# Performance work log

Measured on AMD Instinct MI355X. Metric: run time of the kernel, lower is better.

The kernel has to match this reference:

```python
import jax, jax.numpy as jnp
import numpy as np

N_NODES = 100000
N_EDGES = 1600000
D_IN = 128
D_HID = 128
N_LAYERS = 3


def setup_inputs() -> dict:
    key = jax.random.key(0)
    ks = jax.random.split(key, 7)
    x = jax.random.normal(ks[0], (N_NODES, D_IN), dtype=jnp.float32)
    edge_index = jax.random.randint(ks[1], (2, N_EDGES), 0, N_NODES, dtype=jnp.int32)
    s = 1.0 / np.sqrt(D_HID)
    # stacked per-layer MLP params: lin1 (in->h), lin2 (h->h); in==h==128 for all layers
    W1 = jax.random.uniform(ks[2], (N_LAYERS, D_IN, D_HID), jnp.float32, -s, s)
    b1 = jax.random.uniform(ks[3], (N_LAYERS, D_HID), jnp.float32, -s, s)
    W2 = jax.random.uniform(ks[4], (N_LAYERS, D_HID, D_HID), jnp.float32, -s, s)
    b2 = jax.random.uniform(ks[5], (N_LAYERS, D_HID), jnp.float32, -s, s)
    return {"x": x, "edge_index": edge_index, "W1": W1, "b1": b1, "W2": W2, "b2": b2}


def _gin_layer(x, src, dst, W1, b1, W2, b2):
    # GINConv: out = MLP((1+eps)*x + sum_{j in N(i)} x_j), eps = 0
    agg = jax.ops.segment_sum(x[src], dst, num_segments=N_NODES)  # [N, C]
    h = x + agg
    h = jnp.maximum(h @ W1 + b1, 0.0)  # MLP internal ReLU
    return h @ W2 + b2


def reference(x, edge_index, W1, b1, W2, b2):
    src, dst = edge_index[0], edge_index[1]
    for i in range(N_LAYERS):
        x = _gin_layer(x, src, dst, W1[i], b1[i], W2[i], b2[i])
        if i < N_LAYERS - 1:  # inter-layer act (norm=Identity, dropout=0)
            x = jnp.maximum(x, 0.0)
    return x
```

## Files before the change

### kernel.cpp

```cpp
#include <hip/hip_runtime.h>
#include <hip/hip_bf16.h>

#define D 128

typedef float f32x4 __attribute__((ext_vector_type(4)));
typedef __bf16 bf16x8 __attribute__((ext_vector_type(8)));

__device__ __forceinline__ unsigned short f2bf(float f) {
  unsigned int u = __float_as_uint(f);
  u += 0x7fff + ((u >> 16) & 1);
  return (unsigned short)(u >> 16);
}

__device__ __forceinline__ void gl_lds16(const void* g, void* l) {
  __builtin_amdgcn_global_load_lds(
      (const __attribute__((address_space(1))) unsigned int*)g,
      (__attribute__((address_space(3))) unsigned int*)l, 16, 0, 0);
}

__device__ __forceinline__ int wave_incl_scan(int v, int lane) {
#pragma unroll
  for (int d = 1; d < 64; d <<= 1) {
    int t = __shfl_up(v, d);
    if (lane >= d) v += t;
  }
  return v;
}

#define NBK 196
#define CHUNK 4096

__global__ __launch_bounds__(256) void k_bhist(const int* __restrict__ dst, int E,
                                               int* __restrict__ bcount) {
  __shared__ int cnt[NBK];
  const int tid = threadIdx.x;
  for (int i = tid; i < NBK; i += 256) cnt[i] = 0;
  __syncthreads();
  const int e0 = blockIdx.x * CHUNK;
  const int emax = min(e0 + CHUNK, E);
  for (int e = e0 + tid; e < emax; e += 256)
    atomicAdd(&cnt[((unsigned)dst[e]) >> 9], 1);
  __syncthreads();
  for (int i = tid; i < NBK; i += 256)
    if (cnt[i]) atomicAdd(&bcount[i], cnt[i]);
}

__global__ void k_bscan(const int* __restrict__ bcount, int* __restrict__ bucket_base) {
  int t = threadIdx.x;
  int lane = t & 63, w = t >> 6;
  int v = (t < NBK) ? bcount[t] : 0;
  int s = wave_incl_scan(v, lane);
  __shared__ int ws[4];
  if (lane == 63) ws[w] = s;
  __syncthreads();
  int off = 0;
  for (int i = 0; i < w; i++) off += ws[i];
  if (t < NBK) bucket_base[t] = off + s - v;
  if (t == 0) bucket_base[NBK] = ws[0] + ws[1] + ws[2] + ws[3];
}

__global__ __launch_bounds__(256) void k_binA(const int* __restrict__ src,
                                              const int* __restrict__ dst, int E,
                                              const int* __restrict__ bucket_base,
                                              int* __restrict__ bcursor,
                                              int* __restrict__ pairbuf) {
  __shared__ int cnt[NBK];
  __shared__ int base[NBK];
  const int tid = threadIdx.x;
  const int e0 = blockIdx.x * CHUNK;
  const int emax = min(e0 + CHUNK, E);
  for (int i = tid; i < NBK; i += 256) cnt[i] = 0;
  __syncthreads();
  for (int e = e0 + tid; e < emax; e += 256)
    atomicAdd(&cnt[((unsigned)dst[e]) >> 9], 1);
  __syncthreads();
  for (int i = tid; i < NBK; i += 256) {
    int c = cnt[i];
    int b = 0;
    if (c) b = atomicAdd(&bcursor[i], c) + bucket_base[i];
    base[i] = b;
    cnt[i] = 0;
  }
  __syncthreads();
  for (int e = e0 + tid; e < emax; e += 256) {
    int d = dst[e];
    int bk = ((unsigned)d) >> 9;
    int pos = base[bk] + atomicAdd(&cnt[bk], 1);
    pairbuf[pos] = (src[e] << 9) | (d & 511);
  }
}

#define SEG_CAP 12800
__global__ __launch_bounds__(256) void k_binB(const int* __restrict__ pairbuf,
                                              const int* __restrict__ bucket_base,
                                              int* __restrict__ col,
                                              int* __restrict__ row_ptr, int N) {
  __shared__ int sdeg[512];
  __shared__ int rpl[512];
  __shared__ int cur[512];
  __shared__ int wsum[4];
  __shared__ int stage[SEG_CAP];
  const int tid = threadIdx.x;
  const int lane = tid & 63, wid = tid >> 6;
  const int node0 = blockIdx.x << 9;
  const int nn = min(512, N - node0);
  const int start = bucket_base[blockIdx.x];
  const int end = bucket_base[blockIdx.x + 1];
  const int sz = end - start;
  for (int i = tid; i < 512; i += 256) { sdeg[i] = 0; cur[i] = 0; }
  __syncthreads();
  for (int i = tid; i < sz; i += 256)
    atomicAdd(&sdeg[pairbuf[start + i] & 511], 1);
  __syncthreads();
  int a = sdeg[2 * tid], b = sdeg[2 * tid + 1];
  int v = a + b;
  int s = wave_incl_scan(v, lane);
  if (lane == 63) wsum[wid] = s;
  __syncthreads();
  int off = 0;
  for (int k = 0; k < wid; k++) off += wsum[k];
  int e0l = off + s - v;
  rpl[2 * tid] = e0l;
  rpl[2 * tid + 1] = e0l + a;
  __syncthreads();
  for (int i = tid; i < nn; i += 256) row_ptr[node0 + i] = start + rpl[i];
  if (blockIdx.x == gridDim.x - 1 && tid == 0) row_ptr[N] = end;
  for (int i = tid; i < sz; i += 256) {
    int pk = pairbuf[start + i];
    int d = pk & 511;
    int pos = rpl[d] + atomicAdd(&cur[d], 1);
    if (pos < SEG_CAP) stage[pos] = (int)(((unsigned)pk) >> 9);
  }
  __syncthreads();
  for (int i = tid; i < sz; i += 256) col[start + i] = stage[i];
}

#define ISSUE8(vv, cvh, base)                              \
  _Pragma("unroll") for (int u = 0; u < 8; u++) {          \
    int s_ = __shfl((cvh), (base) + u);                    \
    vv[u] = Yu[(size_t)s_ * 64 + lane];                    \
  }

#define REDUCE8(vv, jb)                                    \
  _Pragma("unroll") for (int u = 0; u < 8; u++) {          \
    float fx_ = __uint_as_float(vv[u] << 16);              \
    float fy_ = __uint_as_float(vv[u] & 0xffff0000u);      \
    if ((jb) + u < degA) { axA += fx_; ayA += fy_; }       \
    else { axB += fx_; ayB += fy_; }                       \
  }

__global__ __launch_bounds__(256) void k_agg(const unsigned short* __restrict__ Y,
                                             const int* __restrict__ row_ptr,
                                             const int* __restrict__ col,
                                             const float* __restrict__ bias,
                                             unsigned short* __restrict__ H, int N) {
  const int pw = (blockIdx.x * 256 + threadIdx.x) >> 6;
  const int lane = threadIdx.x & 63;
  const int nA = pw * 2, nB = nA + 1;
  if (nA >= N) return;
  const bool hasB = (nB < N);
  const unsigned int* Yu = (const unsigned int*)Y;
  unsigned int svA = Yu[(size_t)nA * 64 + lane];
  unsigned int svB = hasB ? Yu[(size_t)nB * 64 + lane] : 0u;
  float2 bv = ((const float2*)bias)[lane];
  int rsA = row_ptr[nA];
  int reA = row_ptr[nA + 1];
  int reB = hasB ? row_ptr[nA + 2] : reA;
  rsA = __builtin_amdgcn_readfirstlane(rsA);
  reA = __builtin_amdgcn_readfirstlane(reA);
  reB = __builtin_amdgcn_readfirstlane(reB);
  const int degA = min(reA - rsA, 64);
  const int degB = min(reB - reA, 64);
  const int m = degA + degB;
  const int mPad = (m + 7) & ~7;
  const int nb = mPad >> 3;

  float axA = bv.x + __uint_as_float(svA << 16);
  float ayA = bv.y + __uint_as_float(svA & 0xffff0000u);
  float axB = bv.x + __uint_as_float(svB << 16);
  float ayB = bv.y + __uint_as_float(svB & 0xffff0000u);

  int cv0 = N, cv1 = N;
  if (lane < degA) cv0 = col[rsA + lane];
  else if (lane - degA < degB) cv0 = col[reA + (lane - degA)];
  if (64 + lane < m) cv1 = col[reA + (64 + lane - degA)];

  unsigned int b0[8], b1[8];
  int issued = 0, done = 0;
  if (nb > 0) { ISSUE8(b0, cv0, 0); issued = 1; }
  if (nb > 1) { ISSUE8(b1, cv0, 8); issued = 2; }
  while (done < nb) {
    if ((done & 1) == 0) { REDUCE8(b0, (done << 3)); }
    else { REDUCE8(b1, (done << 3)); }
    done++;
    if (issued < nb) {
      int ch = (issued < 8) ? cv0 : cv1;
      int bs = (issued & 7) << 3;
      if ((issued & 1) == 0) { ISSUE8(b0, ch, bs); }
      else { ISSUE8(b1, ch, bs); }
      issued++;
    }
  }
  for (int t = rsA + 64; t < reA; t++) {
    unsigned int v = Yu[(size_t)col[t] * 64 + lane];
    axA += __uint_as_float(v << 16);
    ayA += __uint_as_float(v & 0xffff0000u);
  }
  for (int t = reA + 64; t < reB; t++) {
    unsigned int v = Yu[(size_t)col[t] * 64 + lane];
    axB += __uint_as_float(v << 16);
    ayB += __uint_as_float(v & 0xffff0000u);
  }

  unsigned int pA = ((unsigned int)f2bf(fmaxf(ayA, 0.f)) << 16) | f2bf(fmaxf(axA, 0.f));
  ((unsigned int*)H)[(size_t)nA * 64 + lane] = pA;
  if (hasB) {
    unsigned int pB = ((unsigned int)f2bf(fmaxf(ayB, 0.f)) << 16) | f2bf(fmaxf(axB, 0.f));
    ((unsigned int*)H)[(size_t)nB * 64 + lane] = pB;
  }
}

__global__ void k_prep(const float* __restrict__ W1, const float* __restrict__ W2,
                       unsigned short* __restrict__ Wt) {
  int b = blockIdx.x;
  const float* W = (b & 1) ? (W2 + (size_t)(b >> 1) * D * D) : (W1 + (size_t)(b >> 1) * D * D);
  unsigned short* O = Wt + (size_t)b * D * D;
  for (int i = threadIdx.x; i < D * D; i += 256) {
    int n = i >> 7, k = i & 127;
    O[n * D + k] = f2bf(W[k * D + n]);
  }
}

template <bool A_FP32, bool OUT_FP32>
__global__ __launch_bounds__(256) void k_gemm(const void* __restrict__ Ain,
                                              const unsigned short* __restrict__ Wt,
                                              const float* __restrict__ bias,
                                              void* __restrict__ Cout, int M, int relu) {
  __shared__ __align__(16) unsigned short As[64 * 128];
  __shared__ __align__(16) unsigned short Bs[128 * 128];
  const int tid = threadIdx.x;
  const int wid = tid >> 6, lane = tid & 63;
  const int R0 = blockIdx.x * 64;

#pragma unroll
  for (int g = 0; g < 8; g++) {
    int flat = g * 256 + tid;
    int n = flat >> 4, p = flat & 15;
    int l = p ^ (n & 15);
    gl_lds16(Wt + (size_t)n * D + l * 8, &Bs[(size_t)(g * 256 + wid * 64) * 8]);
  }
  if (A_FP32) {
    const float* A = (const float*)Ain;
#pragma unroll
    for (int g = 0; g < 4; g++) {
      int flat = g * 256 + tid;
      int row = flat >> 4, p = flat & 15;
      int l = p ^ (row & 15);
      float4 a0 = make_float4(0.f, 0.f, 0.f, 0.f), a1 = a0;
      if (R0 + row < M) {
        a0 = *(const float4*)(A + (size_t)(R0 + row) * D + l * 8);
        a1 = *(const float4*)(A + (size_t)(R0 + row) * D + l * 8 + 4);
      }
      ushort4 v0, v1;
      v0.x = f2bf(a0.x); v0.y = f2bf(a0.y); v0.z = f2bf(a0.z); v0.w = f2bf(a0.w);
      v1.x = f2bf(a1.x); v1.y = f2bf(a1.y); v1.z = f2bf(a1.z); v1.w = f2bf(a1.w);
      *(ushort4*)&As[row * D + p * 8] = v0;
      *(ushort4*)&As[row * D + p * 8 + 4] = v1;
    }
  } else {
    const unsigned short* A = (const unsigned short*)Ain;
#pragma unroll
    for (int g = 0; g < 4; g++) {
      int flat = g * 256 + tid;
      int row = flat >> 4, p = flat & 15;
      int l = p ^ (row & 15);
      gl_lds16(A + (size_t)(R0 + row) * D + l * 8, &As[(size_t)(g * 256 + wid * 64) * 8]);
    }
  }
  __syncthreads();

  const int wr = wid >> 1, wc = wid & 1;
  const int lm = lane & 15, lq = lane >> 4;
  f32x4 acc[2][4];
#pragma unroll
  for (int i = 0; i < 2; i++)
#pragma unroll
    for (int j = 0; j < 4; j++) acc[i][j] = f32x4{0.f, 0.f, 0.f, 0.f};

#pragma unroll
  for (int kc = 0; kc < 4; kc++) {
    const int pc = (kc * 4 + lq) ^ lm;
    bf16x8 af[2], bfr[4];
#pragma unroll
    for (int i = 0; i < 2; i++)
      af[i] = *(const bf16x8*)&As[(wr * 32 + i * 16 + lm) * D + pc * 8];
#pragma unroll
    for (int j = 0; j < 4; j++)
      bfr[j] = *(const bf16x8*)&Bs[(wc * 64 + j * 16 + lm) * D + pc * 8];
#pragma unroll
    for (int i = 0; i < 2; i++)
#pragma unroll
      for (int j = 0; j < 4; j++)
        acc[i][j] = __builtin_amdgcn_mfma_f32_16x16x32_bf16(af[i], bfr[j], acc[i][j], 0, 0, 0);
  }

  float bv[4];
#pragma unroll
  for (int j = 0; j < 4; j++) bv[j] = bias ? bias[wc * 64 + j * 16 + lm] : 0.f;
#pragma unroll
  for (int i = 0; i < 2; i++) {
#pragma unroll
    for (int reg = 0; reg < 4; reg++) {
      const int gr = R0 + wr * 32 + i * 16 + lq * 4 + reg;
      if (gr < M) {
#pragma unroll
        for (int j = 0; j < 4; j++) {
          const int gc = wc * 64 + j * 16 + lm;
          float v = acc[i][j][reg] + bv[j];
          if (relu) v = fmaxf(v, 0.f);
          if (OUT_FP32)
            ((float*)Cout)[(size_t)gr * D + gc] = v;
          else
            ((unsigned short*)Cout)[(size_t)gr * D + gc] = f2bf(v);
        }
      }
    }
  }
}

__global__ __launch_bounds__(256) void k_gemm2(const unsigned short* __restrict__ Ain,
                                               const unsigned short* __restrict__ W2t,
                                               const unsigned short* __restrict__ W1t,
                                               const float* __restrict__ b2,
                                               unsigned short* __restrict__ Cout, int M) {
  __shared__ __align__(16) unsigned short As[64 * 128];
  __shared__ __align__(16) unsigned short Bs[128 * 128];
  const int tid = threadIdx.x;
  const int wid = tid >> 6, lane = tid & 63;
  const int R0 = blockIdx.x * 64;

#pragma unroll
  for (int g = 0; g < 8; g++) {
    int flat = g * 256 + tid;
    int n = flat >> 4, p = flat & 15;
    int l = p ^ (n & 15);
    gl_lds16(W2t + (size_t)n * D + l * 8, &Bs[(size_t)(g * 256 + wid * 64) * 8]);
  }
#pragma unroll
  for (int g = 0; g < 4; g++) {
    int flat = g * 256 + tid;
    int row = flat >> 4, p = flat & 15;
    int l = p ^ (row & 15);
    gl_lds16(Ain + (size_t)(R0 + row) * D + l * 8, &As[(size_t)(g * 256 + wid * 64) * 8]);
  }
  __syncthreads();

  const int wr = wid >> 1, wc = wid & 1;
  const int lm = lane & 15, lq = lane >> 4;
  f32x4 acc[2][4];
#pragma unroll
  for (int i = 0; i < 2; i++)
#pragma unroll
    for (int j = 0; j < 4; j++) acc[i][j] = f32x4{0.f, 0.f, 0.f, 0.f};
#pragma unroll
  for (int kc = 0; kc < 4; kc++) {
    const int pc = (kc * 4 + lq) ^ lm;
    bf16x8 af[2], bfr[4];
#pragma unroll
    for (int i = 0; i < 2; i++)
      af[i] = *(const bf16x8*)&As[(wr * 32 + i * 16 + lm) * D + pc * 8];
#pragma unroll
    for (int j = 0; j < 4; j++)
      bfr[j] = *(const bf16x8*)&Bs[(wc * 64 + j * 16 + lm) * D + pc * 8];
#pragma unroll
    for (int i = 0; i < 2; i++)
#pragma unroll
      for (int j = 0; j < 4; j++)
        acc[i][j] = __builtin_amdgcn_mfma_f32_16x16x32_bf16(af[i], bfr[j], acc[i][j], 0, 0, 0);
  }
  __syncthreads();

#pragma unroll
  for (int g = 0; g < 8; g++) {
    int flat = g * 256 + tid;
    int n = flat >> 4, p = flat & 15;
    int l = p ^ (n & 15);
    gl_lds16(W1t + (size_t)n * D + l * 8, &Bs[(size_t)(g * 256 + wid * 64) * 8]);
  }
  {
    float bv[4];
#pragma unroll
    for (int j = 0; j < 4; j++) bv[j] = b2[wc * 64 + j * 16 + lm];
#pragma unroll
    for (int i = 0; i < 2; i++) {
#pragma unroll
      for (int reg = 0; reg < 4; reg++) {
        const int row = wr * 32 + i * 16 + lq * 4 + reg;
#pragma unroll
        for (int j = 0; j < 4; j++) {
          const int gc = wc * 64 + j * 16 + lm;
          float v = fmaxf(acc[i][j][reg] + bv[j], 0.f);
          As[row * D + (((gc >> 3) ^ (row & 15)) << 3) + (gc & 7)] = f2bf(v);
        }
      }
    }
  }
  __syncthreads();

  f32x4 acc2[2][4];
#pragma unroll
  for (int i = 0; i < 2; i++)
#pragma unroll
    for (int j = 0; j < 4; j++) acc2[i][j] = f32x4{0.f, 0.f, 0.f, 0.f};
#pragma unroll
  for (int kc = 0; kc < 4; kc++) {
    const int pc = (kc * 4 + lq) ^ lm;
    bf16x8 af[2], bfr[4];
#pragma unroll
    for (int i = 0; i < 2; i++)
      af[i] = *(const bf16x8*)&As[(wr * 32 + i * 16 + lm) * D + pc * 8];
#pragma unroll
    for (int j = 0; j < 4; j++)
      bfr[j] = *(const bf16x8*)&Bs[(wc * 64 + j * 16 + lm) * D + pc * 8];
#pragma unroll
    for (int i = 0; i < 2; i++)
#pragma unroll
      for (int j = 0; j < 4; j++)
        acc2[i][j] = __builtin_amdgcn_mfma_f32_16x16x32_bf16(af[i], bfr[j], acc2[i][j], 0, 0, 0);
  }
#pragma unroll
  for (int i = 0; i < 2; i++) {
#pragma unroll
    for (int reg = 0; reg < 4; reg++) {
      const int gr = R0 + wr * 32 + i * 16 + lq * 4 + reg;
      if (gr < M) {
#pragma unroll
        for (int j = 0; j < 4; j++) {
          const int gc = wc * 64 + j * 16 + lm;
          Cout[(size_t)gr * D + gc] = f2bf(acc2[i][j][reg]);
        }
      }
    }
  }
}

extern "C" void kernel_launch(void* const* d_in, const int* in_sizes, int n_in,
                              void* d_out, int out_size, void* d_ws, size_t ws_size,
                              hipStream_t stream) {
  const float* x  = (const float*)d_in[0];
  const int*   ei = (const int*)d_in[1];
  const float* W1 = (const float*)d_in[2];
  const float* b1 = (const float*)d_in[3];
  const float* W2 = (const float*)d_in[4];
  const float* b2 = (const float*)d_in[5];
  const int N = in_sizes[0] / D;
  const int E = in_sizes[1] / 2;
  const int* src = ei;
  const int* dst = ei + E;

  char* ws = (char*)d_ws;
  unsigned short* Wt   = (unsigned short*)ws;
  unsigned short* bufA = Wt + 6 * D * D;
  unsigned short* bufB = bufA + (size_t)(N + 1) * D;
  int* pairbuf = (int*)bufB;
  int* row_ptr = (int*)(bufB + (size_t)(N + 1) * D);
  int* colv    = row_ptr + (N + 1);
  int* bucket_base = colv + E;
  int* bcount  = bucket_base + 256;
  int* bcursor = bcount + 256;
  float* OUT   = (float*)d_out;

  const int CB = (E + CHUNK - 1) / CHUNK;
  const int GB = (N + 63) / 64;
  const int AB = ((N + 1) / 2 + 3) / 4;
  const int BKB = (N + 511) / 512;

  k_prep<<<6, 256, 0, stream>>>(W1, W2, Wt);
  hipMemsetAsync(bcount, 0, 512 * sizeof(int), stream);
  hipMemsetAsync(bufA + (size_t)N * D, 0, D * sizeof(unsigned short), stream);
  hipMemsetAsync(bufB + (size_t)N * D, 0, D * sizeof(unsigned short), stream);
  k_bhist<<<CB, 256, 0, stream>>>(dst, E, bcount);
  k_bscan<<<1, 256, 0, stream>>>(bcount, bucket_base);
  k_binA<<<CB, 256, 0, stream>>>(src, dst, E, bucket_base, bcursor, pairbuf);
  k_binB<<<BKB, 256, 0, stream>>>(pairbuf, bucket_base, colv, row_ptr, N);

  k_gemm<true, false><<<GB, 256, 0, stream>>>(x, Wt + 0 * D * D, nullptr, bufA, N, 0);
  k_agg<<<AB, 256, 0, stream>>>(bufA, row_ptr, colv, b1, bufB, N);
  k_gemm2<<<GB, 256, 0, stream>>>(bufB, Wt + 1 * D * D, Wt + 2 * D * D, b2, bufA, N);
  k_agg<<<AB, 256, 0, stream>>>(bufA, row_ptr, colv, b1 + D, bufB, N);
  k_gemm2<<<GB, 256, 0, stream>>>(bufB, Wt + 3 * D * D, Wt + 4 * D * D, b2 + D, bufA, N);
  k_agg<<<AB, 256, 0, stream>>>(bufA, row_ptr, colv, b1 + 2 * D, bufB, N);
  k_gemm<false, true><<<GB, 256, 0, stream>>>(bufB, Wt + 5 * D * D, b2 + 2 * D, OUT, N, 0);
  (void)n_in; (void)out_size; (void)ws_size;
}
```

Baseline: 426.9 us.

## Fuse neighbor aggregation into following GEMM kernel and fold scan and memsets

The gather-sum aggregation is moved into the MLP GEMM kernel. Each block aggregates its 64 rows straight into shared memory and then runs the two matmuls, so the bf16 intermediate H no longer makes a round trip through global memory and three kernel launches go away. The separate bucket scan kernel is removed: binA recomputes the prefix scan per block and binB sums bcount itself. The memsets are folded into the prep kernel. The trade-off is less parallelism for the latency-bound gather, with one block per 64 rows instead of many small waves and LDS use limiting occupancy, plus some redundant scan work.

```diff
diff --git a/kernel.cpp b/kernel.cpp
--- a/kernel.cpp
+++ b/kernel.cpp
@@ -45,31 +45,31 @@
     if (cnt[i]) atomicAdd(&bcount[i], cnt[i]);
 }
 
-__global__ void k_bscan(const int* __restrict__ bcount, int* __restrict__ bucket_base) {
-  int t = threadIdx.x;
-  int lane = t & 63, w = t >> 6;
-  int v = (t < NBK) ? bcount[t] : 0;
-  int s = wave_incl_scan(v, lane);
-  __shared__ int ws[4];
-  if (lane == 63) ws[w] = s;
-  __syncthreads();
-  int off = 0;
-  for (int i = 0; i < w; i++) off += ws[i];
-  if (t < NBK) bucket_base[t] = off + s - v;
-  if (t == 0) bucket_base[NBK] = ws[0] + ws[1] + ws[2] + ws[3];
-}
-
 __global__ __launch_bounds__(256) void k_binA(const int* __restrict__ src,
                                               const int* __restrict__ dst, int E,
-                                              const int* __restrict__ bucket_base,
+                                              const int* __restrict__ bcount,
                                               int* __restrict__ bcursor,
                                               int* __restrict__ pairbuf) {
   __shared__ int cnt[NBK];
   __shared__ int base[NBK];
+  __shared__ int bb[NBK];
+  __shared__ int ws4[4];
   const int tid = threadIdx.x;
   const int e0 = blockIdx.x * CHUNK;
   const int emax = min(e0 + CHUNK, E);
   for (int i = tid; i < NBK; i += 256) cnt[i] = 0;
+  {
+    int lane = tid & 63, w = tid >> 6;
+    int v = (tid < NBK) ? bcount[tid] : 0;
+    int s = wave_incl_scan(v, lane);
+    if (lane == 63) ws4[w] = s;
+    __syncthreads();
+    if (tid < NBK) {
+      int off = 0;
+      for (int k = 0; k < w; k++) off += ws4[k];
+      bb[tid] = off + s - v;
+    }
+  }
   __syncthreads();
   for (int e = e0 + tid; e < emax; e += 256)
     atomicAdd(&cnt[((unsigned)dst[e]) >> 9], 1);
@@ -77,7 +77,7 @@
   for (int i = tid; i < NBK; i += 256) {
     int c = cnt[i];
     int b = 0;
-    if (c) b = atomicAdd(&bcursor[i], c) + bucket_base[i];
+    if (c) b = atomicAdd(&bcursor[i], c) + bb[i];
     base[i] = b;
     cnt[i] = 0;
   }
@@ -92,23 +92,31 @@
 
 #define SEG_CAP 12800
 __global__ __launch_bounds__(256) void k_binB(const int* __restrict__ pairbuf,
-                                              const int* __restrict__ bucket_base,
+                                              const int* __restrict__ bcount,
                                               int* __restrict__ col,
                                               int* __restrict__ row_ptr, int N) {
   __shared__ int sdeg[512];
   __shared__ int rpl[512];
   __shared__ int cur[512];
   __shared__ int wsum[4];
+  __shared__ int wsum2[4];
   __shared__ int stage[SEG_CAP];
   const int tid = threadIdx.x;
   const int lane = tid & 63, wid = tid >> 6;
   const int node0 = blockIdx.x << 9;
   const int nn = min(512, N - node0);
-  const int start = bucket_base[blockIdx.x];
-  const int end = bucket_base[blockIdx.x + 1];
+  {
+    int vv = (tid < (int)blockIdx.x) ? bcount[tid] : 0;
+    vv += __shfl_down(vv, 32); vv += __shfl_down(vv, 16);
+    vv += __shfl_down(vv, 8);  vv += __shfl_down(vv, 4);
+    vv += __shfl_down(vv, 2);  vv += __shfl_down(vv, 1);
+    if (lane == 0) wsum2[wid] = vv;
+  }
+  for (int i = tid; i < 512; i += 256) { sdeg[i] = 0; cur[i] = 0; }
+  __syncthreads();
+  const int start = wsum2[0] + wsum2[1] + wsum2[2] + wsum2[3];
+  const int end = start + bcount[blockIdx.x];
   const int sz = end - start;
-  for (int i = tid; i < 512; i += 256) { sdeg[i] = 0; cur[i] = 0; }
-  __syncthreads();
   for (int i = tid; i < sz; i += 256)
     atomicAdd(&sdeg[pairbuf[start + i] & 511], 1);
   __syncthreads();
@@ -135,99 +143,24 @@
   for (int i = tid; i < sz; i += 256) col[start + i] = stage[i];
 }
 
-#define ISSUE8(vv, cvh, base)                              \
-  _Pragma("unroll") for (int u = 0; u < 8; u++) {          \
-    int s_ = __shfl((cvh), (base) + u);                    \
-    vv[u] = Yu[(size_t)s_ * 64 + lane];                    \
-  }
-
-#define REDUCE8(vv, jb)                                    \
-  _Pragma("unroll") for (int u = 0; u < 8; u++) {          \
-    float fx_ = __uint_as_float(vv[u] << 16);              \
-    float fy_ = __uint_as_float(vv[u] & 0xffff0000u);      \
-    if ((jb) + u < degA) { axA += fx_; ayA += fy_; }       \
-    else { axB += fx_; ayB += fy_; }                       \
-  }
-
-__global__ __launch_bounds__(256) void k_agg(const unsigned short* __restrict__ Y,
-                                             const int* __restrict__ row_ptr,
-                                             const int* __restrict__ col,
-                                             const float* __restrict__ bias,
-                                             unsigned short* __restrict__ H, int N) {
-  const int pw = (blockIdx.x * 256 + threadIdx.x) >> 6;
-  const int lane = threadIdx.x & 63;
-  const int nA = pw * 2, nB = nA + 1;
-  if (nA >= N) return;
-  const bool hasB = (nB < N);
-  const unsigned int* Yu = (const unsigned int*)Y;
-  unsigned int svA = Yu[(size_t)nA * 64 + lane];
-  unsigned int svB = hasB ? Yu[(size_t)nB * 64 + lane] : 0u;
-  float2 bv = ((const float2*)bias)[lane];
-  int rsA = row_ptr[nA];
-  int reA = row_ptr[nA + 1];
-  int reB = hasB ? row_ptr[nA + 2] : reA;
-  rsA = __builtin_amdgcn_readfirstlane(rsA);
-  reA = __builtin_amdgcn_readfirstlane(reA);
-  reB = __builtin_amdgcn_readfirstlane(reB);
-  const int degA = min(reA - rsA, 64);
-  const int degB = min(reB - reA, 64);
-  const int m = degA + degB;
-  const int mPad = (m + 7) & ~7;
-  const int nb = mPad >> 3;
-
-  float axA = bv.x + __uint_as_float(svA << 16);
-  float ayA = bv.y + __uint_as_float(svA & 0xffff0000u);
-  float axB = bv.x + __uint_as_float(svB << 16);
-  float ayB = bv.y + __uint_as_float(svB & 0xffff0000u);
-
-  int cv0 = N, cv1 = N;
-  if (lane < degA) cv0 = col[rsA + lane];
-  else if (lane - degA < degB) cv0 = col[reA + (lane - degA)];
-  if (64 + lane < m) cv1 = col[reA + (64 + lane - degA)];
-
-  unsigned int b0[8], b1[8];
-  int issued = 0, done = 0;
-  if (nb > 0) { ISSUE8(b0, cv0, 0); issued = 1; }
-  if (nb > 1) { ISSUE8(b1, cv0, 8); issued = 2; }
-  while (done < nb) {
-    if ((done & 1) == 0) { REDUCE8(b0, (done << 3)); }
-    else { REDUCE8(b1, (done << 3)); }
-    done++;
-    if (issued < nb) {
-      int ch = (issued < 8) ? cv0 : cv1;
-      int bs = (issued & 7) << 3;
-      if ((issued & 1) == 0) { ISSUE8(b0, ch, bs); }
-      else { ISSUE8(b1, ch, bs); }
-      issued++;
-    }
-  }
-  for (int t = rsA + 64; t < reA; t++) {
-    unsigned int v = Yu[(size_t)col[t] * 64 + lane];
-    axA += __uint_as_float(v << 16);
-    ayA += __uint_as_float(v & 0xffff0000u);
-  }
-  for (int t = reA + 64; t < reB; t++) {
-    unsigned int v = Yu[(size_t)col[t] * 64 + lane];
-    axB += __uint_as_float(v << 16);
-    ayB += __uint_as_float(v & 0xffff0000u);
-  }
-
-  unsigned int pA = ((unsigned int)f2bf(fmaxf(ayA, 0.f)) << 16) | f2bf(fmaxf(axA, 0.f));
-  ((unsigned int*)H)[(size_t)nA * 64 + lane] = pA;
-  if (hasB) {
-    unsigned int pB = ((unsigned int)f2bf(fmaxf(ayB, 0.f)) << 16) | f2bf(fmaxf(axB, 0.f));
-    ((unsigned int*)H)[(size_t)nB * 64 + lane] = pB;
-  }
-}
-
 __global__ void k_prep(const float* __restrict__ W1, const float* __restrict__ W2,
-                       unsigned short* __restrict__ Wt) {
+                       unsigned short* __restrict__ Wt, int* __restrict__ bcount,
+                       unsigned short* __restrict__ padA, unsigned short* __restrict__ padB) {
   int b = blockIdx.x;
-  const float* W = (b & 1) ? (W2 + (size_t)(b >> 1) * D * D) : (W1 + (size_t)(b >> 1) * D * D);
-  unsigned short* O = Wt + (size_t)b * D * D;
-  for (int i = threadIdx.x; i < D * D; i += 256) {
-    int n = i >> 7, k = i & 127;
-    O[n * D + k] = f2bf(W[k * D + n]);
+  if (b < 6) {
+    const float* W = (b & 1) ? (W2 + (size_t)(b >> 1) * D * D) : (W1 + (size_t)(b >> 1) * D * D);
+    unsigned short* O = Wt + (size_t)b * D * D;
+    for (int i = threadIdx.x; i < D * D; i += 256) {
+      int n = i >> 7, k = i & 127;
+      O[n * D + k] = f2bf(W[k * D + n]);
+    }
+  } else if (b == 6) {
+    for (int i = threadIdx.x; i < 512; i += 256) bcount[i] = 0;
+  } else {
+    if (threadIdx.x < 64) {
+      ((unsigned int*)padA)[threadIdx.x] = 0u;
+      ((unsigned int*)padB)[threadIdx.x] = 0u;
+    }
   }
 }
 
@@ -328,11 +261,26 @@
   }
 }
 
-__global__ __launch_bounds__(256) void k_gemm2(const unsigned short* __restrict__ Ain,
-                                               const unsigned short* __restrict__ W2t,
-                                               const unsigned short* __restrict__ W1t,
-                                               const float* __restrict__ b2,
-                                               unsigned short* __restrict__ Cout, int M) {
+#define ISSUE8(vv, cvh, base)                              \
+  _Pragma("unroll") for (int u = 0; u < 8; u++) {          \
+    int s_ = __shfl((cvh), (base) + u);                    \
+    vv[u] = Yu[(size_t)s_ * 64 + lane];                    \
+  }
+
+#define REDUCE8(vv, jb)                                    \
+  _Pragma("unroll") for (int u = 0; u < 8; u++) {          \
+    float fx_ = __uint_as_float(vv[u] << 16);              \
+    float fy_ = __uint_as_float(vv[u] & 0xffff0000u);      \
+    if ((jb) + u < degA) { axA += fx_; ayA += fy_; }       \
+    else { axB += fx_; ayB += fy_; }                       \
+  }
+
+template <bool FINAL>
+__global__ __launch_bounds__(256) void k_aggemm(
+    const unsigned short* __restrict__ Y, const int* __restrict__ row_ptr,
+    const int* __restrict__ col, const float* __restrict__ b1,
+    const unsigned short* __restrict__ Wa, const unsigned short* __restrict__ Wb,
+    const float* __restrict__ b2, void* __restrict__ Cout, int N) {
   __shared__ __align__(16) unsigned short As[64 * 128];
   __shared__ __align__(16) unsigned short Bs[128 * 128];
   const int tid = threadIdx.x;
@@ -344,14 +292,72 @@
     int flat = g * 256 + tid;
     int n = flat >> 4, p = flat & 15;
     int l = p ^ (n & 15);
-    gl_lds16(W2t + (size_t)n * D + l * 8, &Bs[(size_t)(g * 256 + wid * 64) * 8]);
-  }
-#pragma unroll
-  for (int g = 0; g < 4; g++) {
-    int flat = g * 256 + tid;
-    int row = flat >> 4, p = flat & 15;
-    int l = p ^ (row & 15);
-    gl_lds16(Ain + (size_t)(R0 + row) * D + l * 8, &As[(size_t)(g * 256 + wid * 64) * 8]);
+    gl_lds16(Wa + (size_t)n * D + l * 8, &Bs[(size_t)(g * 256 + wid * 64) * 8]);
+  }
+
+  const unsigned int* Yu = (const unsigned int*)Y;
+  unsigned int* Asu = (unsigned int*)As;
+  const float2 bv = ((const float2*)b1)[lane];
+
+  for (int pi = 0; pi < 8; pi++) {
+    const int r0 = wid * 16 + pi * 2;
+    const int nA = R0 + r0, nB = nA + 1;
+    const int wA = r0 * 64 + (((lane >> 2) ^ (r0 & 15)) << 2) + (lane & 3);
+    const int wB = (r0 + 1) * 64 + (((lane >> 2) ^ ((r0 + 1) & 15)) << 2) + (lane & 3);
+    if (nA >= N) { Asu[wA] = 0u; Asu[wB] = 0u; continue; }
+    const bool hasB = (nB < N);
+    unsigned int svA = Yu[(size_t)nA * 64 + lane];
+    unsigned int svB = hasB ? Yu[(size_t)nB * 64 + lane] : 0u;
+    int rsA = row_ptr[nA];
+    int reA = row_ptr[nA + 1];
+    int reB = hasB ? row_ptr[nA + 2] : reA;
+    rsA = __builtin_amdgcn_readfirstlane(rsA);
+    reA = __builtin_amdgcn_readfirstlane(reA);
+    reB = __builtin_amdgcn_readfirstlane(reB);
+    const int degA = min(reA - rsA, 64);
+    const int degB = min(reB - reA, 64);
+    const int m = degA + degB;
+    const int nb = (m + 7) >> 3;
+
+    float axA = bv.x + __uint_as_float(svA << 16);
+    float ayA = bv.y + __uint_as_float(svA & 0xffff0000u);
+    float axB = bv.x + __uint_as_float(svB << 16);
+    float ayB = bv.y + __uint_as_float(svB & 0xffff0000u);
+
+    int cv0 = N, cv1 = N;
+    if (lane < degA) cv0 = col[rsA + lane];
+    else if (lane - degA < degB) cv0 = col[reA + (lane - degA)];
+    if (64 + lane < m) cv1 = col[reA + (64 + lane - degA)];
+
+    unsigned int g0[8], g1[8];
+    int issued = 0, done = 0;
+    if (nb > 0) { ISSUE8(g0, cv0, 0); issued = 1; }
+    if (nb > 1) { ISSUE8(g1, cv0, 8); issued = 2; }
+    while (done < nb) {
+      if ((done & 1) == 0) { REDUCE8(g0, (done << 3)); }
+      else { REDUCE8(g1, (done << 3)); }
+      done++;
+      if (issued < nb) {
+        int ch = (issued < 8) ? cv0 : cv1;
+        int bs = (issued & 7) << 3;
+        if ((issued & 1) == 0) { ISSUE8(g0, ch, bs); }
+        else { ISSUE8(g1, ch, bs); }
+        issued++;
+      }
+    }
+    for (int t = rsA + 64; t < reA; t++) {
+      unsigned int v = Yu[(size_t)col[t] * 64 + lane];
+      axA += __uint_as_float(v << 16);
+      ayA += __uint_as_float(v & 0xffff0000u);
+    }
+    for (int t = reA + 64; t < reB; t++) {
+      unsigned int v = Yu[(size_t)col[t] * 64 + lane];
+      axB += __uint_as_float(v << 16);
+      ayB += __uint_as_float(v & 0xffff0000u);
+    }
+    Asu[wA] = ((unsigned int)f2bf(fmaxf(ayA, 0.f)) << 16) | f2bf(fmaxf(axA, 0.f));
+    Asu[wB] = hasB ? (((unsigned int)f2bf(fmaxf(ayB, 0.f)) << 16) | f2bf(fmaxf(axB, 0.f)))
+                   : 0u;
   }
   __syncthreads();
 
@@ -378,66 +384,86 @@
       for (int j = 0; j < 4; j++)
         acc[i][j] = __builtin_amdgcn_mfma_f32_16x16x32_bf16(af[i], bfr[j], acc[i][j], 0, 0, 0);
   }
-  __syncthreads();
-
-#pragma unroll
-  for (int g = 0; g < 8; g++) {
-    int flat = g * 256 + tid;
-    int n = flat >> 4, p = flat & 15;
-    int l = p ^ (n & 15);
-    gl_lds16(W1t + (size_t)n * D + l * 8, &Bs[(size_t)(g * 256 + wid * 64) * 8]);
-  }
-  {
-    float bv[4];
-#pragma unroll
-    for (int j = 0; j < 4; j++) bv[j] = b2[wc * 64 + j * 16 + lm];
+
+  if (FINAL) {
+    float bvv[4];
+#pragma unroll
+    for (int j = 0; j < 4; j++) bvv[j] = b2[wc * 64 + j * 16 + lm];
 #pragma unroll
     for (int i = 0; i < 2; i++) {
 #pragma unroll
       for (int reg = 0; reg < 4; reg++) {
-        const int row = wr * 32 + i * 16 + lq * 4 + reg;
-#pragma unroll
-        for (int j = 0; j < 4; j++) {
-          const int gc = wc * 64 + j * 16 + lm;
-          float v = fmaxf(acc[i][j][reg] + bv[j], 0.f);
-          As[row * D + (((gc >> 3) ^ (row & 15)) << 3) + (gc & 7)] = f2bf(v);
+        const int gr = R0 + wr * 32 + i * 16 + lq * 4 + reg;
+        if (gr < N) {
+#pragma unroll
+          for (int j = 0; j < 4; j++) {
+            const int gc = wc * 64 + j * 16 + lm;
+            ((float*)Cout)[(size_t)gr * D + gc] = acc[i][j][reg] + bvv[j];
+          }
         }
       }
     }
-  }
-  __syncthreads();
-
-  f32x4 acc2[2][4];
-#pragma unroll
-  for (int i = 0; i < 2; i++)
-#pragma unroll
-    for (int j = 0; j < 4; j++) acc2[i][j] = f32x4{0.f, 0.f, 0.f, 0.f};
-#pragma unroll
-  for (int kc = 0; kc < 4; kc++) {
-    const int pc = (kc * 4 + lq) ^ lm;
-    bf16x8 af[2], bfr[4];
+  } else {
+    __syncthreads();
+#pragma unroll
+    for (int g = 0; g < 8; g++) {
+      int flat = g * 256 + tid;
+      int n = flat >> 4, p = flat & 15;
+      int l = p ^ (n & 15);
+      gl_lds16(Wb + (size_t)n * D + l * 8, &Bs[(size_t)(g * 256 + wid * 64) * 8]);
+    }
+    {
+      float bvv[4];
+#pragma unroll
+      for (int j = 0; j < 4; j++) bvv[j] = b2[wc * 64 + j * 16 + lm];
+#pragma unroll
+      for (int i = 0; i < 2; i++) {
+#pragma unroll
+        for (int reg = 0; reg < 4; reg++) {
+          const int row = wr * 32 + i * 16 + lq * 4 + reg;
+#pragma unroll
+          for (int j = 0; j < 4; j++) {
+            const int gc = wc * 64 + j * 16 + lm;
+            float v = fmaxf(acc[i][j][reg] + bvv[j], 0.f);
+            As[row * D + (((gc >> 3) ^ (row & 15)) << 3) + (gc & 7)] = f2bf(v);
+          }
+        }
+      }
+    }
+    __syncthreads();
+
+    f32x4 acc2[2][4];
 #pragma unroll
     for (int i = 0; i < 2; i++)
-      af[i] = *(const bf16x8*)&As[(wr * 32 + i * 16 + lm) * D + pc * 8];
-#pragma unroll
-    for (int j = 0; j < 4; j++)
-      bfr[j] = *(const bf16x8*)&Bs[(wc * 64 + j * 16 + lm) * D + pc * 8];
-#pragma unroll
-    for (int i = 0; i < 2; i++)
+#pragma unroll
+      for (int j = 0; j < 4; j++) acc2[i][j] = f32x4{0.f, 0.f, 0.f, 0.f};
+#pragma unroll
+    for (int kc = 0; kc < 4; kc++) {
+      const int pc = (kc * 4 + lq) ^ lm;
+      bf16x8 af[2], bfr[4];
+#pragma unroll
+      for (int i = 0; i < 2; i++)
+        af[i] = *(const bf16x8*)&As[(wr * 32 + i * 16 + lm) * D + pc * 8];
 #pragma unroll
       for (int j = 0; j < 4; j++)
-        acc2[i][j] = __builtin_amdgcn_mfma_f32_16x16x32_bf16(af[i], bfr[j], acc2[i][j], 0, 0, 0);
-  }
-#pragma unroll
-  for (int i = 0; i < 2; i++) {
-#pragma unroll
-    for (int reg = 0; reg < 4; reg++) {
-      const int gr = R0 + wr * 32 + i * 16 + lq * 4 + reg;
-      if (gr < M) {
-#pragma unroll
-        for (int j = 0; j < 4; j++) {
-          const int gc = wc * 64 + j * 16 + lm;
-          Cout[(size_t)gr * D + gc] = f2bf(acc2[i][j][reg]);
+        bfr[j] = *(const bf16x8*)&Bs[(wc * 64 + j * 16 + lm) * D + pc * 8];
+#pragma unroll
+      for (int i = 0; i < 2; i++)
+#pragma unroll
+        for (int j = 0; j < 4; j++)
+          acc2[i][j] = __builtin_amdgcn_mfma_f32_16x16x32_bf16(af[i], bfr[j], acc2[i][j], 0, 0, 0);
+    }
+#pragma unroll
+    for (int i = 0; i < 2; i++) {
+#pragma unroll
+      for (int reg = 0; reg < 4; reg++) {
+        const int gr = R0 + wr * 32 + i * 16 + lq * 4 + reg;
+        if (gr < N) {
+#pragma unroll
+          for (int j = 0; j < 4; j++) {
+            const int gc = wc * 64 + j * 16 + lm;
+            ((unsigned short*)Cout)[(size_t)gr * D + gc] = f2bf(acc2[i][j][reg]);
+          }
         }
       }
     }
@@ -465,31 +491,26 @@
   int* pairbuf = (int*)bufB;
   int* row_ptr = (int*)(bufB + (size_t)(N + 1) * D);
   int* colv    = row_ptr + (N + 1);
-  int* bucket_base = colv + E;
-  int* bcount  = bucket_base + 256;
+  int* bcount  = colv + E;
   int* bcursor = bcount + 256;
   float* OUT   = (float*)d_out;
 
   const int CB = (E + CHUNK - 1) / CHUNK;
   const int GB = (N + 63) / 64;
-  const int AB = ((N + 1) / 2 + 3) / 4;
   const int BKB = (N + 511) / 512;
 
-  k_prep<<<6, 256, 0, stream>>>(W1, W2, Wt);
-  hipMemsetAsync(bcount, 0, 512 * sizeof(int), stream);
-  hipMemsetAsync(bufA + (size_t)N * D, 0, D * sizeof(unsigned short), stream);
-  hipMemsetAsync(bufB + (size_t)N * D, 0, D * sizeof(unsigned short), stream);
+  k_prep<<<8, 256, 0, stream>>>(W1, W2, Wt, bcount,
+                                bufA + (size_t)N * D, bufB + (size_t)N * D);
   k_bhist<<<CB, 256, 0, stream>>>(dst, E, bcount);
-  k_bscan<<<1, 256, 0, stream>>>(bcount, bucket_base);
-  k_binA<<<CB, 256, 0, stream>>>(src, dst, E, bucket_base, bcursor, pairbuf);
-  k_binB<<<BKB, 256, 0, stream>>>(pairbuf, bucket_base, colv, row_ptr, N);
+  k_binA<<<CB, 256, 0, stream>>>(src, dst, E, bcount, bcursor, pairbuf);
+  k_binB<<<BKB, 256, 0, stream>>>(pairbuf, bcount, colv, row_ptr, N);
 
   k_gemm<true, false><<<GB, 256, 0, stream>>>(x, Wt + 0 * D * D, nullptr, bufA, N, 0);
-  k_agg<<<AB, 256, 0, stream>>>(bufA, row_ptr, colv, b1, bufB, N);
-  k_gemm2<<<GB, 256, 0, stream>>>(bufB, Wt + 1 * D * D, Wt + 2 * D * D, b2, bufA, N);
-  k_agg<<<AB, 256, 0, stream>>>(bufA, row_ptr, colv, b1 + D, bufB, N);
-  k_gemm2<<<GB, 256, 0, stream>>>(bufB, Wt + 3 * D * D, Wt + 4 * D * D, b2 + D, bufA, N);
-  k_agg<<<AB, 256, 0, stream>>>(bufA, row_ptr, colv, b1 + 2 * D, bufB, N);
-  k_gemm<false, true><<<GB, 256, 0, stream>>>(bufB, Wt + 5 * D * D, b2 + 2 * D, OUT, N, 0);
+  k_aggemm<false><<<GB, 256, 0, stream>>>(bufA, row_ptr, colv, b1,
+                                          Wt + 1 * D * D, Wt + 2 * D * D, b2, bufB, N);
+  k_aggemm<false><<<GB, 256, 0, stream>>>(bufB, row_ptr, colv, b1 + D,
+                                          Wt + 3 * D * D, Wt + 4 * D * D, b2 + D, bufA, N);
+  k_aggemm<true><<<GB, 256, 0, stream>>>(bufA, row_ptr, colv, b1 + 2 * D,
+                                         Wt + 5 * D * D, nullptr, b2 + 2 * D, OUT, N);
   (void)n_in; (void)out_size; (void)ws_size;
 }
```

Measured after the change: 538.8 us. +26.2%, slower.
